# Performance work log

Measured on AMD Instinct MI355X. Metric: run time of the kernel, lower is better.

Reference implementation:

```python
import jax, jax.numpy as jnp
import numpy as np

HEADS, KDIM, VDIM = 8, 32, 64  # ImageLinearAttention defaults
EPS = 1e-8

def lrelu(x):
    return jax.nn.leaky_relu(x, 0.2)

def up2(x):
    # torch nn.Upsample(scale_factor=2, mode='bilinear', align_corners=False)
    b, c, h, w = x.shape
    return jax.image.resize(x, (b, c, 2 * h, 2 * w), method='bilinear')

def blur(x):
    # normalized [1,2,1] outer-product depthwise blur (kornia filter2d, normalized=True)
    c = x.shape[1]
    f = jnp.array([1.0, 2.0, 1.0], dtype=x.dtype)
    k = (f[:, None] * f[None, :]) / 16.0
    kern = jnp.broadcast_to(k, (c, 1, 3, 3))
    return jax.lax.conv_general_dilated(x, kern, (1, 1), [(1, 1), (1, 1)], feature_group_count=c)

def conv2dmod(x, W, y, demod):
    # x [b,ci,h,w], W [co,ci,k,k], y [b,ci]; per-sample modulated (de)conv
    w = W[None] * (y[:, None, :, None, None] + 1.0)  # [b,co,ci,k,k]
    if demod:
        d = jax.lax.rsqrt(jnp.sum(w * w, axis=(2, 3, 4), keepdims=True) + EPS)
        w = w * d
    pad = (W.shape[-1] - 1) // 2  # same padding, stride=1, dilation=1
    conv1 = lambda xi, wi: jax.lax.conv_general_dilated(xi[None], wi, (1, 1), [(pad, pad), (pad, pad)])[0]
    return jax.vmap(conv1)(x, w)

def attn_and_ff(x, qw, kw, vw, ow, ob, ga, f1w, f1b, f2w, f2b, gf):
    # Residual(Rezero(ImageLinearAttention)) then Residual(Rezero(conv1x1-leaky-conv1x1))
    b, c, h, w = x.shape
    n = h * w
    xf = x.reshape(b, c, n)
    scale = KDIM ** -0.25
    q = (jnp.einsum('dc,bcn->bdn', qw, xf) * scale).reshape(b, HEADS, KDIM, n)
    k = (jnp.einsum('dc,bcn->bdn', kw, xf) * scale).reshape(b, HEADS, KDIM, n)
    v = jnp.einsum('dc,bcn->bdn', vw, xf).reshape(b, HEADS, VDIM, n)
    k = jax.nn.softmax(k, axis=-1)          # over pixels
    q = jax.nn.softmax(q, axis=-2)          # norm_queries: over key dim
    ctx = jnp.einsum('bhdn,bhen->bhde', k, v)
    out = jnp.einsum('bhdn,bhde->bhen', q, ctx).reshape(b, HEADS * VDIM, n)
    out = jnp.einsum('cd,bdn->bcn', ow, out) + ob[None, :, None]
    x = x + ga * out.reshape(b, c, h, w)
    h1 = lrelu(jnp.einsum('dc,bcn->bdn', f1w, x.reshape(b, c, n)) + f1b[None, :, None])
    ff = jnp.einsum('cd,bdn->bcn', f2w, h1) + f2b[None, :, None]
    return x + gf * ff.reshape(b, c, h, w)

def setup_inputs() -> dict:
    key = jax.random.key(0)
    ks = jax.random.split(key, 20)
    B, CIN, F, L, H, W = 4, 128, 64, 512, 64, 64
    DK, DV = HEADS * KDIM, HEADS * VDIM
    d = {}
    d['x'] = jax.random.normal(ks[0], (B, CIN, H, W), jnp.float32)
    d['prev_rgb'] = jax.random.normal(ks[1], (B, 3, 2 * H, 2 * W), jnp.float32)
    d['istyle'] = jax.random.normal(ks[2], (B, L), jnp.float32)
    d['noise1'] = jax.random.normal(ks[3], (B, F, 2 * H, 2 * W), jnp.float32)
    d['noise2'] = jax.random.normal(ks[4], (B, F, 2 * H, 2 * W), jnp.float32)
    d['conv1_w'] = jax.random.normal(ks[5], (F, CIN, 3, 3), jnp.float32) * (2.0 / (CIN * 9)) ** 0.5
    d['conv2_w'] = jax.random.normal(ks[6], (F, F, 3, 3), jnp.float32) * (2.0 / (F * 9)) ** 0.5
    d['style_w'] = jax.random.normal(ks[7], (F, L), jnp.float32) * L ** -0.5
    d['style_b'] = jnp.zeros((F,), jnp.float32)
    d['rgb_w'] = jax.random.normal(ks[8], (3, F, 1, 1), jnp.float32) * (2.0 / F) ** 0.5
    d['qw'] = jax.random.normal(ks[9], (2, DK, F), jnp.float32) * F ** -0.5
    d['kw'] = jax.random.normal(ks[10], (2, DK, F), jnp.float32) * F ** -0.5
    d['vw'] = jax.random.normal(ks[11], (2, DV, F), jnp.float32) * F ** -0.5
    d['ow'] = jax.random.normal(ks[12], (2, F, DV), jnp.float32) * DV ** -0.5
    d['ob'] = jnp.zeros((2, F), jnp.float32)
    d['ga'] = 0.1 * jnp.ones((2,), jnp.float32)  # rezero gate (nonzero for a meaningful baseline)
    d['f1w'] = jax.random.normal(ks[13], (2, 2 * F, F), jnp.float32) * F ** -0.5
    d['f1b'] = jnp.zeros((2, 2 * F), jnp.float32)
    d['f2w'] = jax.random.normal(ks[14], (2, F, 2 * F), jnp.float32) * (2 * F) ** -0.5
    d['f2b'] = jnp.zeros((2, F), jnp.float32)
    d['gf'] = 0.1 * jnp.ones((2,), jnp.float32)
    return d

def reference(x, prev_rgb, istyle, noise1, noise2, conv1_w, conv2_w, style_w, style_b, rgb_w,
              qw, kw, vw, ow, ob, ga, f1w, f1b, f2w, f2b, gf):
    b = x.shape[0]
    x = up2(x)
    n1 = attn_and_ff(noise1, qw[0], kw[0], vw[0], ow[0], ob[0], ga[0], f1w[0], f1b[0], f2w[0], f2b[0], gf[0])
    n2 = attn_and_ff(noise2, qw[1], kw[1], vw[1], ow[1], ob[1], ga[1], f1w[1], f1b[1], f2w[1], f2b[1], gf[1])
    ones1 = jnp.ones((b, conv1_w.shape[1]), x.dtype)  # style1 = ones
    x = lrelu(conv2dmod(x, conv1_w, ones1, True) + n1)
    ones2 = jnp.ones((b, conv2_w.shape[1]), x.dtype)  # style2 = ones
    x = lrelu(conv2dmod(x, conv2_w, ones2, True) + n2)
    style = istyle @ style_w.T + style_b             # RGBBlock.to_style
    rgb = conv2dmod(x, rgb_w, style, False) + prev_rgb
    rgb = blur(up2(rgb))                             # upsample_rgb: bilinear x2 + blur
    return (x, rgb)
```

## Files before the change

### kernel.cpp

```cpp
#include <hip/hip_runtime.h>
#include <math.h>

#define NB 4
#define NF 64
#define NPIX 16384
#define DK 256
#define DV 512
#define QKSCALE 0.4204482f

typedef __attribute__((ext_vector_type(8))) short bf16x8;
typedef __attribute__((ext_vector_type(4))) float f32x4;
#define MFMA16(a, b, c) __builtin_amdgcn_mfma_f32_16x16x32_bf16(a, b, c, 0, 0, 0)

__device__ __forceinline__ short f2bf(float f) {
  unsigned u = __builtin_bit_cast(unsigned, f);
  unsigned r = (u + 0x7FFFu + ((u >> 16) & 1u)) >> 16;
  return (short)r;
}
__device__ __forceinline__ float bf2f(short s) {
  unsigned u = ((unsigned)(unsigned short)s) << 16;
  return __builtin_bit_cast(float, u);
}

#define OFF_XUPT   0L
#define OFF_XAT    4194304L
#define OFF_NBT    6291456L
#define OFF_NZT    10485760L
#define OFF_GPART  14680064L
#define OFF_WB1    25165824L
#define OFF_WB2    25202688L
#define OFF_STYLE  25221120L
#define OFF_RGBS   25221376L
#define OFF_QWB    25417984L
#define OFF_KWB    25434368L
#define OFF_F1WB   25450752L
#define OFF_F2WB   25458944L
#define OFF_MTT    25467136L

#define CDIV(a,b) (((a)+(b)-1)/(b))

__global__ void cvt4_kernel(const float* __restrict__ qw, const float* __restrict__ kw,
                            const float* __restrict__ f1w, const float* __restrict__ f2w,
                            short* __restrict__ qwP, short* __restrict__ kwP,
                            short* __restrict__ f1P, short* __restrict__ f2P) {
  int i = blockIdx.x * 256 + threadIdx.x;
  if (i < 32768) {
    int i_t = i >> 14, rem = i & 16383;
    int hd = rem >> 10, ks = (rem >> 9) & 1, lane = (rem >> 3) & 63, j = rem & 7;
    int l15 = lane & 15, quad = lane >> 4;
    qwP[i] = f2bf(qw[i_t * 16384 + (hd * 16 + l15) * 64 + ks * 32 + quad * 8 + j]);
  } else if (i < 65536) {
    int ii = i - 32768;
    int i_t = ii >> 14, rem = ii & 16383;
    int q = rem >> 12, dt = (rem >> 10) & 3, ks = (rem >> 9) & 1, lane = (rem >> 3) & 63, j = rem & 7;
    int l15 = lane & 15, quad = lane >> 4;
    kwP[ii] = f2bf(kw[i_t * 16384 + (q * 64 + dt * 16 + l15) * 64 + ks * 32 + quad * 8 + j]);
  } else if (i < 81920) {
    int ii = i - 65536;
    int i_t = ii >> 13, rem = ii & 8191;
    int jt = rem >> 10, ks = (rem >> 9) & 1, lane = (rem >> 3) & 63, j = rem & 7;
    int l15 = lane & 15, quad = lane >> 4;
    f1P[ii] = f2bf(f1w[i_t * 8192 + (jt * 16 + l15) * 64 + ks * 32 + quad * 8 + j]);
  } else {
    int ii = i - 81920;
    int i_t = ii >> 13, rem = ii & 8191;
    int ct = rem >> 11, p = (rem >> 10) & 1, ks = (rem >> 9) & 1, lane = (rem >> 3) & 63, j = rem & 7;
    int l15 = lane & 15, quad = lane >> 4;
    f2P[ii] = f2bf(f2w[i_t * 8192 + (ct * 16 + l15) * 128 + p * 64 + ks * 32 + quad * 8 + j]);
  }
}

__global__ __launch_bounds__(256) void up2t_kernel(const float* __restrict__ in,
                                                   short* __restrict__ outT) {
  __shared__ float row[64 * 132];
  int b = blockIdx.y, y = blockIdx.x, tid = threadIdx.x;
  float iy = y * 0.5f - 0.25f;
  int y0 = (int)floorf(iy); float wy = iy - (float)y0;
  int ylo = y0 < 0 ? 0 : y0;
  int yhi = y0 + 1 > 63 ? 63 : y0 + 1;
  for (int it = 0; it < 32; ++it) {
    int idx = it * 256 + tid;
    int c = idx >> 6, xin = idx & 63;
    const float* bp = in + ((long)(b * 128 + c)) * 4096;
    float v0 = bp[ylo * 64 + xin];
    float v1 = bp[yhi * 64 + xin];
    row[xin * 132 + c] = (1.f - wy) * v0 + wy * v1;
  }
  __syncthreads();
  int x = tid >> 1, c0 = (tid & 1) * 64;
  float ix = x * 0.5f - 0.25f;
  int x0 = (int)floorf(ix); float wx = ix - (float)x0;
  int xlo = x0 < 0 ? 0 : x0;
  int xhi = x0 + 1 > 63 ? 63 : x0 + 1;
  long obase = (((long)(b * 128 + y)) * 128 + x) * 128 + c0;
#pragma unroll
  for (int i = 0; i < 8; ++i) {
    bf16x8 pack;
#pragma unroll
    for (int r = 0; r < 8; ++r) {
      int c = c0 + i * 8 + r;
      float v = (1.f - wx) * row[xlo * 132 + c] + wx * row[xhi * 132 + c];
      pack[r] = f2bf(v);
    }
    *(bf16x8*)(outT + obase + i * 8) = pack;
  }
}

__global__ __launch_bounds__(256) void nzt_kernel(const float* __restrict__ nz1,
                                                  const float* __restrict__ nz2,
                                                  short* __restrict__ nzP) {
  __shared__ short tile[64 * 65];
  int i = blockIdx.z, b = blockIdx.y;
  long n0 = (long)blockIdx.x * 64;
  const float* nz = (i == 0) ? nz1 : nz2;
  int tid = threadIdx.x;
  const float* src = nz + (long)b * 64 * NPIX + n0;
#pragma unroll
  for (int k = 0; k < 16; ++k) {
    int idx = tid + k * 256;
    int n = idx & 63, c = idx >> 6;
    tile[c * 65 + n] = f2bf(src[(long)c * NPIX + n]);
  }
  __syncthreads();
  long fragb = ((long)(i * NB + b)) * 1024 + blockIdx.x * 4;
#pragma unroll
  for (int v = 0; v < 2; ++v) {
    int vid = tid + v * 256;
    int ntl = vid >> 7, ks = (vid >> 6) & 1, lane = vid & 63;
    int l15 = lane & 15, quad = lane >> 4;
    bf16x8 pack;
#pragma unroll
    for (int j = 0; j < 8; ++j)
      pack[j] = tile[(ks * 32 + quad * 8 + j) * 65 + ntl * 16 + l15];
    *(bf16x8*)(nzP + ((fragb + ntl) * 2 + ks) * 512 + lane * 8) = pack;
  }
}

__global__ void wnormT_kernel(const float* __restrict__ W, short* __restrict__ wbP, int CI) {
  int co = blockIdx.x;
  int n = CI * 9;
  int KS = CI >> 5;
  __shared__ float red[256];
  float s = 0.f;
  for (int idx = threadIdx.x; idx < n; idx += 256) {
    float w2 = 2.0f * W[co * n + idx];
    s += w2 * w2;
  }
  red[threadIdx.x] = s;
  __syncthreads();
  for (int off = 128; off > 0; off >>= 1) {
    if (threadIdx.x < off) red[threadIdx.x] += red[threadIdx.x + off];
    __syncthreads();
  }
  float sc = rsqrtf(red[0] + 1e-8f);
  int ct = co >> 4, l15 = co & 15;
  for (int idx = threadIdx.x; idx < n; idx += 256) {
    int ci = idx / 9, k = idx - ci * 9;
    int ks = ci >> 5, quad = (ci >> 3) & 3, j = ci & 7;
    wbP[((k * 4 + ct) * KS + ks) * 512 + (quad * 16 + l15) * 8 + j] =
        f2bf(2.0f * W[co * n + idx] * sc);
  }
}

__global__ void style_kernel(const float* __restrict__ istyle, const float* __restrict__ sw,
                             const float* __restrict__ sb, float* __restrict__ styleb) {
  int b = threadIdx.x >> 6;
  int c = threadIdx.x & 63;
  float a = 0.f;
  const float* ip = istyle + b * 512;
  const float* wp = sw + c * 512;
  for (int l = 0; l < 512; ++l) a += ip[l] * wp[l];
  styleb[b * 64 + c] = a + sb[c];
}

__global__ __launch_bounds__(256, 2) void pk_kernel(const float* __restrict__ nz1,
                                                    const float* __restrict__ nz2,
                                                    const short* __restrict__ kwP,
                                                    short* __restrict__ Gpartb) {
  __shared__ __attribute__((aligned(16))) char lds[57600];
  int bi = blockIdx.x, ch = blockIdx.y;
  int i = bi >> 2, b = bi & 3;
  const float* nz = (i == 0) ? nz1 : nz2;
  const short* kwP_i = kwP + i * (DK * NF);
  int tid = threadIdx.x;
  int w = tid >> 6, lane = tid & 63, quad = lane >> 4, l15 = lane & 15;
  int n0 = ch * 128;
  short* Xb = (short*)lds;
  short* Xt = (short*)(lds + 21760);
  short* Ph = (short*)(lds + 40192);
  for (int k = 0; k < 32; ++k) {
    int idx = tid + k * 256;
    int c = idx >> 7, n = idx & 127;
    float v = nz[((long)b * 64 + c) * NPIX + n0 + n];
    short bv = f2bf(v);
    Xb[c * 136 + n] = bv;
    Xt[n * 72 + c] = bv;
  }
  for (int k = 0; k < 8; ++k) {
    int idx = tid + k * 256;
    int c = 64 + (idx >> 7), n = idx & 127;
    Xb[c * 136 + n] = (c == 64) ? (short)0x3F80 : (short)0;
  }
  __syncthreads();
  for (int q = 0; q < 4; ++q) {
    f32x4 acc[2][4];
#pragma unroll
    for (int j = 0; j < 2; ++j)
#pragma unroll
      for (int dt = 0; dt < 4; ++dt) acc[j][dt] = (f32x4){0.f, 0.f, 0.f, 0.f};
#pragma unroll
    for (int j = 0; j < 2; ++j) {
      int ntile = 2 * w + j;
#pragma unroll
      for (int ks = 0; ks < 2; ++ks) {
        bf16x8 bfr = *(const bf16x8*)(Xt + (ntile * 16 + l15) * 72 + ks * 32 + quad * 8);
#pragma unroll
        for (int dt = 0; dt < 4; ++dt) {
          bf16x8 afr = *(const bf16x8*)(kwP_i + (((q * 4 + dt) * 2 + ks) * 512 + lane * 8));
          acc[j][dt] = MFMA16(afr, bfr, acc[j][dt]);
        }
      }
    }
#pragma unroll
    for (int j = 0; j < 2; ++j) {
      int ntile = 2 * w + j;
#pragma unroll
      for (int dt = 0; dt < 4; ++dt)
#pragma unroll
        for (int r = 0; r < 4; ++r) {
          float p = __expf(acc[j][dt][r] * QKSCALE);
          Ph[(dt * 16 + quad * 4 + r) * 136 + ntile * 16 + l15] = f2bf(p);
        }
    }
    __syncthreads();
#pragma unroll
    for (int ct = 0; ct < 5; ++ct) {
      f32x4 g = (f32x4){0.f, 0.f, 0.f, 0.f};
#pragma unroll
      for (int ks = 0; ks < 4; ++ks) {
        bf16x8 afr = *(const bf16x8*)(Ph + (w * 16 + l15) * 136 + ks * 32 + quad * 8);
        bf16x8 bfr = *(const bf16x8*)(Xb + (ct * 16 + l15) * 136 + ks * 32 + quad * 8);
        g = MFMA16(afr, bfr, g);
      }
#pragma unroll
      for (int r = 0; r < 4; ++r) {
        int row = q * 64 + w * 16 + quad * 4 + r;
        Gpartb[(((long)bi * 128 + ch) * 256 + row) * 80 + ct * 16 + l15] = f2bf(g[r]);
      }
    }
    __syncthreads();
  }
}

__global__ __launch_bounds__(256) void ctxM_kernel(const short* __restrict__ Gpartb,
                                                   const float* __restrict__ vw,
                                                   const float* __restrict__ ow,
                                                   short* __restrict__ MtP) {
  int i = blockIdx.z, b = blockIdx.y, dt = blockIdx.x * 16;
  int h = dt >> 5;
  __shared__ float Gs[16][81];
  __shared__ float ctxs[16][68];
  int t = threadIdx.x;
  const short* gb = Gpartb + ((long)(i * NB + b)) * 128 * 256 * 80;
  if (t < 160) {
    int dl = t / 10, c8 = t % 10;
    float acc[8] = {0.f, 0.f, 0.f, 0.f, 0.f, 0.f, 0.f, 0.f};
    const short* gp = gb + ((long)(dt + dl)) * 80 + c8 * 8;
    for (int ch = 0; ch < 128; ++ch) {
      bf16x8 v = *(const bf16x8*)(gp + (long)ch * 20480);
#pragma unroll
      for (int r = 0; r < 8; ++r) acc[r] += bf2f(v[r]);
    }
#pragma unroll
    for (int r = 0; r < 8; ++r) Gs[dl][c8 * 8 + r] = acc[r];
  }
  __syncthreads();
  const float* vw_i = vw + (long)i * DV * NF;
  const float* ow_i = ow + (long)i * NF * DV;
  for (int idx = t; idx < 1024; idx += 256) {
    int dl = idx & 15, e = idx >> 4;
    const float* vp = vw_i + (h * 64 + e) * 64;
    float a = 0.f;
#pragma unroll
    for (int c = 0; c < 64; ++c) a += Gs[dl][c] * vp[c];
    ctxs[dl][e] = a / Gs[dl][64];
  }
  __syncthreads();
  short* mtp = MtP + ((long)(i * NB + b)) * 16384;
  for (int idx = t; idx < 1024; idx += 256) {
    int dl = idx & 15, c = idx >> 4;
    const float* op = ow_i + c * 512 + h * 64;
    float a = 0.f;
#pragma unroll
    for (int e = 0; e < 64; ++e) a += op[e] * ctxs[dl][e];
    int d = dt + dl;
    int ct = c >> 4, l15 = c & 15, hh = d >> 5, quad = (d >> 3) & 3, r = d & 7;
    mtp[((ct * 8 + hh) * 64 + quad * 16 + l15) * 8 + r] = f2bf(a);
  }
}

__global__ __launch_bounds__(256, 6) void attnd4_kernel(
    const short* __restrict__ nzP, const short* __restrict__ qwP,
    const short* __restrict__ MtP, const float* __restrict__ ob,
    const float* __restrict__ gap, const short* __restrict__ f1P,
    const float* __restrict__ f1b, const short* __restrict__ f2P,
    const float* __restrict__ f2b, const float* __restrict__ gfp,
    short* __restrict__ noutP) {
  __shared__ __attribute__((aligned(16))) short lds[4 * 2048];
  int bi = blockIdx.x;
  int i = bi >> 2, b = bi & 3;
  (void)b;
  int tid = threadIdx.x;
  int w = tid >> 6, lane = tid & 63, quad = lane >> 4, l15 = lane & 15;
  short* Xt = lds + w * 2048;
  short* Es = Xt + 1152;
  float ga = gap[i], gf = gfp[i];
  const short* qwP_i = qwP + i * (DK * NF);
  const short* f1P_i = f1P + i * (128 * 64);
  const float* f1b_i = f1b + i * 128;
  const short* f2P_i = f2P + i * (64 * 128);
  const float* f2b_i = f2b + i * 64;
  const float* ob_i = ob + i * 64;
  long ntile = (long)bi * 1024 + blockIdx.y * 4 + w;
  const short* nb = nzP + ntile * 1024;
  bf16x8 xfr0 = *(const bf16x8*)(nb + lane * 8);
  bf16x8 xfr1 = *(const bf16x8*)(nb + 512 + lane * 8);
  *(bf16x8*)(Xt + l15 * 72 + quad * 8) = xfr0;
  *(bf16x8*)(Xt + l15 * 72 + 32 + quad * 8) = xfr1;
  const short* mtp = MtP + (long)bi * 16384;
  f32x4 acc2[4];
#pragma unroll
  for (int ct = 0; ct < 4; ++ct) acc2[ct] = (f32x4){0.f, 0.f, 0.f, 0.f};
#pragma unroll
  for (int h = 0; h < 8; ++h) {
    f32x4 q[2];
#pragma unroll
    for (int dd = 0; dd < 2; ++dd) {
      int hd = 2 * h + dd;
      q[dd] = (f32x4){0.f, 0.f, 0.f, 0.f};
      bf16x8 a0 = *(const bf16x8*)(qwP_i + (hd * 2 + 0) * 512 + lane * 8);
      q[dd] = MFMA16(a0, xfr0, q[dd]);
      bf16x8 a1 = *(const bf16x8*)(qwP_i + (hd * 2 + 1) * 512 + lane * 8);
      q[dd] = MFMA16(a1, xfr1, q[dd]);
    }
    float part = 0.f;
#pragma unroll
    for (int dd = 0; dd < 2; ++dd)
#pragma unroll
      for (int r = 0; r < 4; ++r) {
        float e = __expf(q[dd][r] * QKSCALE);
        q[dd][r] = e;
        part += e;
      }
    float p2 = part + __shfl_xor(part, 16);
    float s = p2 + __shfl_xor(p2, 32);
    float inv = 1.0f / s;
#pragma unroll
    for (int dd = 0; dd < 2; ++dd) {
      short4 ev;
      ev.x = f2bf(q[dd][0] * inv); ev.y = f2bf(q[dd][1] * inv);
      ev.z = f2bf(q[dd][2] * inv); ev.w = f2bf(q[dd][3] * inv);
      *(short4*)(Es + l15 * 56 + dd * 16 + quad * 4) = ev;
    }
    bf16x8 efr = *(const bf16x8*)(Es + l15 * 56 + quad * 8);
#pragma unroll
    for (int ct = 0; ct < 4; ++ct) {
      bf16x8 afr = *(const bf16x8*)(mtp + (ct * 8 + h) * 512 + lane * 8);
      acc2[ct] = MFMA16(afr, efr, acc2[ct]);
    }
  }
  float yreg[4][4];
#pragma unroll
  for (int ct = 0; ct < 4; ++ct) {
    int c0 = ct * 16 + quad * 4;
    short4 xs = *(const short4*)(Xt + l15 * 72 + c0);
    float xv[4] = {bf2f(xs.x), bf2f(xs.y), bf2f(xs.z), bf2f(xs.w)};
    short4 ys;
#pragma unroll
    for (int r = 0; r < 4; ++r) yreg[ct][r] = xv[r] + ga * (acc2[ct][r] + ob_i[c0 + r]);
    ys.x = f2bf(yreg[ct][0]); ys.y = f2bf(yreg[ct][1]);
    ys.z = f2bf(yreg[ct][2]); ys.w = f2bf(yreg[ct][3]);
    *(short4*)(Xt + l15 * 72 + c0) = ys;
  }
  bf16x8 yfr0 = *(const bf16x8*)(Xt + l15 * 72 + quad * 8);
  bf16x8 yfr1 = *(const bf16x8*)(Xt + l15 * 72 + 32 + quad * 8);
  f32x4 acc3[8];
#pragma unroll
  for (int jt = 0; jt < 8; ++jt) {
    acc3[jt] = (f32x4){0.f, 0.f, 0.f, 0.f};
    bf16x8 a0 = *(const bf16x8*)(f1P_i + (jt * 2 + 0) * 512 + lane * 8);
    acc3[jt] = MFMA16(a0, yfr0, acc3[jt]);
    bf16x8 a1 = *(const bf16x8*)(f1P_i + (jt * 2 + 1) * 512 + lane * 8);
    acc3[jt] = MFMA16(a1, yfr1, acc3[jt]);
  }
  f32x4 acc4[4];
#pragma unroll
  for (int ct = 0; ct < 4; ++ct) acc4[ct] = (f32x4){0.f, 0.f, 0.f, 0.f};
#pragma unroll
  for (int p = 0; p < 2; ++p) {
#pragma unroll
    for (int jj = 0; jj < 4; ++jj) {
      int jt = p * 4 + jj;
      short4 hs;
#pragma unroll
      for (int r = 0; r < 4; ++r) {
        float a = acc3[jt][r] + f1b_i[jt * 16 + quad * 4 + r];
        a = a > 0.f ? a : 0.2f * a;
        ((short*)&hs)[r] = f2bf(a);
      }
      *(short4*)(Xt + l15 * 72 + jj * 16 + quad * 4) = hs;
    }
    bf16x8 h0 = *(const bf16x8*)(Xt + l15 * 72 + quad * 8);
    bf16x8 h1 = *(const bf16x8*)(Xt + l15 * 72 + 32 + quad * 8);
#pragma unroll
    for (int ct = 0; ct < 4; ++ct) {
      bf16x8 a0 = *(const bf16x8*)(f2P_i + ((ct * 2 + p) * 2 + 0) * 512 + lane * 8);
      acc4[ct] = MFMA16(a0, h0, acc4[ct]);
      bf16x8 a1 = *(const bf16x8*)(f2P_i + ((ct * 2 + p) * 2 + 1) * 512 + lane * 8);
      acc4[ct] = MFMA16(a1, h1, acc4[ct]);
    }
  }
#pragma unroll
  for (int ct = 0; ct < 4; ++ct) {
    int c0 = ct * 16 + quad * 4;
    short4 ov;
#pragma unroll
    for (int r = 0; r < 4; ++r)
      ((short*)&ov)[r] = f2bf(yreg[ct][r] + gf * (acc4[ct][r] + f2b_i[c0 + r]));
    *(short4*)(noutP + (ntile * 4 + ct) * 256 + lane * 4) = ov;
  }
}

__global__ __launch_bounds__(256, 4) void convmfma_kernel(
    const short* __restrict__ inT, int CI, const short* __restrict__ wbP,
    const short* __restrict__ addnP, float* __restrict__ out_nchw,
    short* __restrict__ out_nhwc, const float* __restrict__ rgbw,
    const float* __restrict__ styleb, const float* __restrict__ prev,
    float* __restrict__ rgbs) {
  __shared__ __attribute__((aligned(16))) short Bs[3 * 66 * 40];
  int xh = blockIdx.x, y = blockIdx.y, b = blockIdx.z;
  int tid = threadIdx.x;
  int w = tid >> 6, lane = tid & 63, quad = lane >> 4, l15 = lane & 15;
  int KS = CI >> 5;
  f32x4 acc[4];
#pragma unroll
  for (int ct = 0; ct < 4; ++ct) acc[ct] = (f32x4){0.f, 0.f, 0.f, 0.f};
  for (int ks = 0; ks < KS; ++ks) {
    if (ks) __syncthreads();
    for (int t = tid; t < 792; t += 256) {
      int ci8 = t & 3, xr = t >> 2;
      int xi = xr % 66, r = xr / 66;
      int gy = y + r - 1, gx = xh * 64 + xi - 1;
      bf16x8 v = {0, 0, 0, 0, 0, 0, 0, 0};
      if (gy >= 0 && gy < 128 && gx >= 0 && gx < 128)
        v = *(const bf16x8*)(inT + (((long)(b * 128 + gy)) * 128 + gx) * CI + ks * 32 + ci8 * 8);
      *(bf16x8*)(Bs + (r * 66 + xi) * 40 + ci8 * 8) = v;
    }
    __syncthreads();
#pragma unroll
    for (int sh = 0; sh < 9; ++sh) {
      int dyv = sh / 3, dxv = sh - dyv * 3;
      const short* wbase = wbP + ((sh * 4) * KS + ks) * 512 + lane * 8;
      bf16x8 a0 = *(const bf16x8*)(wbase);
      bf16x8 a1 = *(const bf16x8*)(wbase + KS * 512);
      bf16x8 a2 = *(const bf16x8*)(wbase + 2 * KS * 512);
      bf16x8 a3 = *(const bf16x8*)(wbase + 3 * KS * 512);
      int xi = w * 16 + l15 + dxv;
      bf16x8 bf = *(const bf16x8*)(Bs + (dyv * 66 + xi) * 40 + quad * 8);
      acc[0] = MFMA16(a0, bf, acc[0]);
      acc[1] = MFMA16(a1, bf, acc[1]);
      acc[2] = MFMA16(a2, bf, acc[2]);
      acc[3] = MFMA16(a3, bf, acc[3]);
    }
  }
  int x = xh * 64 + w * 16 + l15;
  long nidx = ((long)(b * 128 + y)) * 128 + x;
  long ntile = (long)b * 1024 + y * 8 + xh * 4 + w;
  float p0 = 0.f, p1 = 0.f, p2 = 0.f;
#pragma unroll
  for (int ct = 0; ct < 4; ++ct) {
    short4 ad = *(const short4*)(addnP + (ntile * 4 + ct) * 256 + lane * 4);
    float av[4] = {bf2f(ad.x), bf2f(ad.y), bf2f(ad.z), bf2f(ad.w)};
    float v[4];
#pragma unroll
    for (int r = 0; r < 4; ++r) {
      float a = acc[ct][r] + av[r];
      v[r] = a > 0.f ? a : 0.2f * a;
    }
    if (out_nchw) {
#pragma unroll
      for (int r = 0; r < 4; ++r) {
        int co = ct * 16 + quad * 4 + r;
        out_nchw[((long)(b * 64 + co)) * 16384 + y * 128 + x] = v[r];
      }
    }
    if (out_nhwc) {
      short4 pv;
      pv.x = f2bf(v[0]); pv.y = f2bf(v[1]); pv.z = f2bf(v[2]); pv.w = f2bf(v[3]);
      *(short4*)(out_nhwc + nidx * 64 + ct * 16 + quad * 4) = pv;
    }
    if (rgbw) {
#pragma unroll
      for (int r = 0; r < 4; ++r) {
        int co = ct * 16 + quad * 4 + r;
        float mv = (styleb[b * 64 + co] + 1.0f) * v[r];
        p0 += rgbw[co] * mv;
        p1 += rgbw[64 + co] * mv;
        p2 += rgbw[128 + co] * mv;
      }
    }
  }
  if (rgbw) {
    p0 += __shfl_xor(p0, 16); p0 += __shfl_xor(p0, 32);
    p1 += __shfl_xor(p1, 16); p1 += __shfl_xor(p1, 32);
    p2 += __shfl_xor(p2, 16); p2 += __shfl_xor(p2, 32);
    if (quad == 0) {
      long pi = y * 128 + x;
      rgbs[((long)(b * 3 + 0)) * 16384 + pi] = p0 + prev[((long)(b * 3 + 0)) * 16384 + pi];
      rgbs[((long)(b * 3 + 1)) * 16384 + pi] = p1 + prev[((long)(b * 3 + 1)) * 16384 + pi];
      rgbs[((long)(b * 3 + 2)) * 16384 + pi] = p2 + prev[((long)(b * 3 + 2)) * 16384 + pi];
    }
  }
}

__global__ void upblur_kernel(const float* __restrict__ rgbs, float* __restrict__ out) {
  __shared__ float rows[3][128];
  int bc = blockIdx.y, Y = blockIdx.x, X = threadIdx.x;
  int m = Y >> 1;
  const float* base = rgbs + (long)bc * 16384;
  for (int t = X; t < 384; t += 256) {
    int sr = t >> 7, xx = t & 127;
    int rr = m - 1 + sr;
    rr = rr < 0 ? 0 : (rr > 127 ? 127 : rr);
    rows[sr][xx] = base[rr * 128 + xx];
  }
  __syncthreads();
  const float w3[3] = {1.f, 2.f, 1.f};
  float s = 0.f;
#pragma unroll
  for (int dy = -1; dy <= 1; ++dy) {
    int Yv = Y + dy;
    if (Yv < 0 || Yv > 255) continue;
    float iy = Yv * 0.5f - 0.25f;
    int y0 = (int)floorf(iy); float wy = iy - (float)y0;
    int ylo = y0 < 0 ? 0 : y0;
    int yhi = y0 + 1 > 127 ? 127 : y0 + 1;
    int slo = ylo - m + 1, shi = yhi - m + 1;
#pragma unroll
    for (int dx = -1; dx <= 1; ++dx) {
      int Xv = X + dx;
      if (Xv < 0 || Xv > 255) continue;
      float ix = Xv * 0.5f - 0.25f;
      int x0 = (int)floorf(ix); float wx = ix - (float)x0;
      int xlo = x0 < 0 ? 0 : x0;
      int xhi = x0 + 1 > 127 ? 127 : x0 + 1;
      float v = (1.f - wy) * ((1.f - wx) * rows[slo][xlo] + wx * rows[slo][xhi])
              + wy * ((1.f - wx) * rows[shi][xlo] + wx * rows[shi][xhi]);
      s += w3[dy + 1] * w3[dx + 1] * v;
    }
  }
  out[(long)bc * 65536 + Y * 256 + X] = s * (1.0f / 16.0f);
}

extern "C" void kernel_launch(void* const* d_in, const int* in_sizes, int n_in,
                              void* d_out, int out_size, void* d_ws, size_t ws_size,
                              hipStream_t stream) {
  (void)in_sizes; (void)n_in; (void)out_size; (void)ws_size;
  const float* x        = (const float*)d_in[0];
  const float* prev_rgb = (const float*)d_in[1];
  const float* istyle   = (const float*)d_in[2];
  const float* noise1   = (const float*)d_in[3];
  const float* noise2   = (const float*)d_in[4];
  const float* conv1_w  = (const float*)d_in[5];
  const float* conv2_w  = (const float*)d_in[6];
  const float* style_w  = (const float*)d_in[7];
  const float* style_b  = (const float*)d_in[8];
  const float* rgb_w    = (const float*)d_in[9];
  const float* qw       = (const float*)d_in[10];
  const float* kw       = (const float*)d_in[11];
  const float* vw       = (const float*)d_in[12];
  const float* ow       = (const float*)d_in[13];
  const float* ob       = (const float*)d_in[14];
  const float* ga       = (const float*)d_in[15];
  const float* f1w      = (const float*)d_in[16];
  const float* f1b      = (const float*)d_in[17];
  const float* f2w      = (const float*)d_in[18];
  const float* f2b      = (const float*)d_in[19];
  const float* gf       = (const float*)d_in[20];
  float* out_x   = (float*)d_out;
  float* out_rgb = out_x + 4194304;
  float* ws = (float*)d_ws;

  short* xupT   = (short*)(ws + OFF_XUPT);
  short* xaT    = (short*)(ws + OFF_XAT);
  short* nbufP  = (short*)(ws + OFF_NBT);
  short* nzP    = (short*)(ws + OFF_NZT);
  short* Gpartb = (short*)(ws + OFF_GPART);
  short* wb1    = (short*)(ws + OFF_WB1);
  short* wb2    = (short*)(ws + OFF_WB2);
  float* styleb = ws + OFF_STYLE;
  float* rgbs   = ws + OFF_RGBS;
  short* qwP    = (short*)(ws + OFF_QWB);
  short* kwP    = (short*)(ws + OFF_KWB);
  short* f1P    = (short*)(ws + OFF_F1WB);
  short* f2P    = (short*)(ws + OFF_F2WB);
  short* MtP    = (short*)(ws + OFF_MTT);

  cvt4_kernel<<<384, 256, 0, stream>>>(qw, kw, f1w, f2w, qwP, kwP, f1P, f2P);
  wnormT_kernel<<<64, 256, 0, stream>>>(conv1_w, wb1, 128);
  wnormT_kernel<<<64, 256, 0, stream>>>(conv2_w, wb2, 64);
  style_kernel<<<1, 256, 0, stream>>>(istyle, style_w, style_b, styleb);
  up2t_kernel<<<dim3(128, NB), 256, 0, stream>>>(x, xupT);
  nzt_kernel<<<dim3(256, NB, 2), 256, 0, stream>>>(noise1, noise2, nzP);

  pk_kernel<<<dim3(8, 128), 256, 0, stream>>>(noise1, noise2, kwP, Gpartb);
  ctxM_kernel<<<dim3(16, NB, 2), 256, 0, stream>>>(Gpartb, vw, ow, MtP);
  attnd4_kernel<<<dim3(8, 256), 256, 0, stream>>>(nzP, qwP, MtP, ob, ga,
                                                  f1P, f1b, f2P, f2b, gf, nbufP);

  convmfma_kernel<<<dim3(2, 128, NB), 256, 0, stream>>>(
      xupT, 128, wb1, nbufP, nullptr, xaT, nullptr, nullptr, nullptr, nullptr);
  convmfma_kernel<<<dim3(2, 128, NB), 256, 0, stream>>>(
      xaT, 64, wb2, nbufP + 4194304L, out_x, nullptr, rgb_w, styleb, prev_rgb, rgbs);

  upblur_kernel<<<dim3(256, 12), 256, 0, stream>>>(rgbs, out_rgb);
}
```

Baseline: 309.7 us.

## Split partial-Gram reduction into wide gsum kernel and load pk B-fragments from nzP

The cross-chunk reduction of the 128 partial Gram matrices was done inside ctxM_kernel by only 160 threads per block across 128 blocks. It now runs in a separate gsum_kernel with 163840 threads writing fp32 sums, and ctxM just loads them. pk_kernel also drops its transposed LDS copy of the noise tile. It reads the pre-packed nzP fragments straight into registers, cutting LDS to allow 4 blocks per CU. The cost is one extra launch and an extra fp32 intermediate buffer.

```diff
diff --git a/kernel.cpp b/kernel.cpp
--- a/kernel.cpp
+++ b/kernel.cpp
@@ -36,6 +36,7 @@
 #define OFF_F1WB   25450752L
 #define OFF_F2WB   25458944L
 #define OFF_MTT    25467136L
+#define OFF_GSUM   25532672L
 
 #define CDIV(a,b) (((a)+(b)-1)/(b))
 
@@ -173,11 +174,12 @@
   styleb[b * 64 + c] = a + sb[c];
 }
 
-__global__ __launch_bounds__(256, 2) void pk_kernel(const float* __restrict__ nz1,
+__global__ __launch_bounds__(256, 4) void pk_kernel(const float* __restrict__ nz1,
                                                     const float* __restrict__ nz2,
+                                                    const short* __restrict__ nzP,
                                                     const short* __restrict__ kwP,
                                                     short* __restrict__ Gpartb) {
-  __shared__ __attribute__((aligned(16))) char lds[57600];
+  __shared__ __attribute__((aligned(16))) char lds[39168];
   int bi = blockIdx.x, ch = blockIdx.y;
   int i = bi >> 2, b = bi & 3;
   const float* nz = (i == 0) ? nz1 : nz2;
@@ -186,21 +188,24 @@
   int w = tid >> 6, lane = tid & 63, quad = lane >> 4, l15 = lane & 15;
   int n0 = ch * 128;
   short* Xb = (short*)lds;
-  short* Xt = (short*)(lds + 21760);
-  short* Ph = (short*)(lds + 40192);
+  short* Ph = (short*)(lds + 21760);
   for (int k = 0; k < 32; ++k) {
     int idx = tid + k * 256;
     int c = idx >> 7, n = idx & 127;
-    float v = nz[((long)b * 64 + c) * NPIX + n0 + n];
-    short bv = f2bf(v);
-    Xb[c * 136 + n] = bv;
-    Xt[n * 72 + c] = bv;
+    Xb[c * 136 + n] = f2bf(nz[((long)b * 64 + c) * NPIX + n0 + n]);
   }
   for (int k = 0; k < 8; ++k) {
     int idx = tid + k * 256;
     int c = 64 + (idx >> 7), n = idx & 127;
     Xb[c * 136 + n] = (c == 64) ? (short)0x3F80 : (short)0;
   }
+  bf16x8 bfr[2][2];
+#pragma unroll
+  for (int j = 0; j < 2; ++j)
+#pragma unroll
+    for (int ks = 0; ks < 2; ++ks)
+      bfr[j][ks] = *(const bf16x8*)(nzP +
+          (((long)bi * 1024 + ch * 8 + 2 * w + j) * 2 + ks) * 512 + lane * 8);
   __syncthreads();
   for (int q = 0; q < 4; ++q) {
     f32x4 acc[2][4];
@@ -210,14 +215,12 @@
       for (int dt = 0; dt < 4; ++dt) acc[j][dt] = (f32x4){0.f, 0.f, 0.f, 0.f};
 #pragma unroll
     for (int j = 0; j < 2; ++j) {
-      int ntile = 2 * w + j;
 #pragma unroll
       for (int ks = 0; ks < 2; ++ks) {
-        bf16x8 bfr = *(const bf16x8*)(Xt + (ntile * 16 + l15) * 72 + ks * 32 + quad * 8);
 #pragma unroll
         for (int dt = 0; dt < 4; ++dt) {
           bf16x8 afr = *(const bf16x8*)(kwP_i + (((q * 4 + dt) * 2 + ks) * 512 + lane * 8));
-          acc[j][dt] = MFMA16(afr, bfr, acc[j][dt]);
+          acc[j][dt] = MFMA16(afr, bfr[j][ks], acc[j][dt]);
         }
       }
     }
@@ -239,8 +242,8 @@
 #pragma unroll
       for (int ks = 0; ks < 4; ++ks) {
         bf16x8 afr = *(const bf16x8*)(Ph + (w * 16 + l15) * 136 + ks * 32 + quad * 8);
-        bf16x8 bfr = *(const bf16x8*)(Xb + (ct * 16 + l15) * 136 + ks * 32 + quad * 8);
-        g = MFMA16(afr, bfr, g);
+        bf16x8 bfr2 = *(const bf16x8*)(Xb + (ct * 16 + l15) * 136 + ks * 32 + quad * 8);
+        g = MFMA16(afr, bfr2, g);
       }
 #pragma unroll
       for (int r = 0; r < 4; ++r) {
@@ -252,7 +255,19 @@
   }
 }
 
-__global__ __launch_bounds__(256) void ctxM_kernel(const short* __restrict__ Gpartb,
+__global__ __launch_bounds__(256) void gsum_kernel(const short* __restrict__ Gpartb,
+                                                   float* __restrict__ Gsum) {
+  long idx = (long)blockIdx.x * 256 + threadIdx.x;
+  int bi = (int)(idx / 20480);
+  int rem = (int)(idx % 20480);
+  const short* gp = Gpartb + (long)bi * 128 * 20480 + rem;
+  float s = 0.f;
+#pragma unroll 8
+  for (int ch = 0; ch < 128; ++ch) s += bf2f(gp[(long)ch * 20480]);
+  Gsum[idx] = s;
+}
+
+__global__ __launch_bounds__(256) void ctxM_kernel(const float* __restrict__ Gsum,
                                                    const float* __restrict__ vw,
                                                    const float* __restrict__ ow,
                                                    short* __restrict__ MtP) {
@@ -261,18 +276,10 @@
   __shared__ float Gs[16][81];
   __shared__ float ctxs[16][68];
   int t = threadIdx.x;
-  const short* gb = Gpartb + ((long)(i * NB + b)) * 128 * 256 * 80;
-  if (t < 160) {
-    int dl = t / 10, c8 = t % 10;
-    float acc[8] = {0.f, 0.f, 0.f, 0.f, 0.f, 0.f, 0.f, 0.f};
-    const short* gp = gb + ((long)(dt + dl)) * 80 + c8 * 8;
-    for (int ch = 0; ch < 128; ++ch) {
-      bf16x8 v = *(const bf16x8*)(gp + (long)ch * 20480);
-#pragma unroll
-      for (int r = 0; r < 8; ++r) acc[r] += bf2f(v[r]);
-    }
-#pragma unroll
-    for (int r = 0; r < 8; ++r) Gs[dl][c8 * 8 + r] = acc[r];
+  const float* gsb = Gsum + ((long)(i * NB + b)) * 20480;
+  for (int idx = t; idx < 1280; idx += 256) {
+    int dl = idx / 80, c = idx - dl * 80;
+    Gs[dl][c] = gsb[(dt + dl) * 80 + c];
   }
   __syncthreads();
   const float* vw_i = vw + (long)i * DV * NF;
@@ -308,8 +315,7 @@
     short* __restrict__ noutP) {
   __shared__ __attribute__((aligned(16))) short lds[4 * 2048];
   int bi = blockIdx.x;
-  int i = bi >> 2, b = bi & 3;
-  (void)b;
+  int i = bi >> 2;
   int tid = threadIdx.x;
   int w = tid >> 6, lane = tid & 63, quad = lane >> 4, l15 = lane & 15;
   short* Xt = lds + w * 2048;
@@ -605,6 +611,7 @@
   short* f1P    = (short*)(ws + OFF_F1WB);
   short* f2P    = (short*)(ws + OFF_F2WB);
   short* MtP    = (short*)(ws + OFF_MTT);
+  float* Gsum   = ws + OFF_GSUM;
 
   cvt4_kernel<<<384, 256, 0, stream>>>(qw, kw, f1w, f2w, qwP, kwP, f1P, f2P);
   wnormT_kernel<<<64, 256, 0, stream>>>(conv1_w, wb1, 128);
@@ -613,8 +620,9 @@
   up2t_kernel<<<dim3(128, NB), 256, 0, stream>>>(x, xupT);
   nzt_kernel<<<dim3(256, NB, 2), 256, 0, stream>>>(noise1, noise2, nzP);
 
-  pk_kernel<<<dim3(8, 128), 256, 0, stream>>>(noise1, noise2, kwP, Gpartb);
-  ctxM_kernel<<<dim3(16, NB, 2), 256, 0, stream>>>(Gpartb, vw, ow, MtP);
+  pk_kernel<<<dim3(8, 128), 256, 0, stream>>>(noise1, noise2, nzP, kwP, Gpartb);
+  gsum_kernel<<<640, 256, 0, stream>>>(Gpartb, Gsum);
+  ctxM_kernel<<<dim3(16, NB, 2), 256, 0, stream>>>(Gsum, vw, ow, MtP);
   attnd4_kernel<<<dim3(8, 256), 256, 0, stream>>>(nzP, qwP, MtP, ob, ga,
                                                   f1P, f1b, f2P, f2b, gf, nbufP);
 
```

After: 306.5 us. Within noise of the previous version (-1.0%).
